# Kernel tuning notes

Hardware: AMD Instinct MI355X
Metric: run time of the kernel (lower is better)

## Reference

```python
import jax, jax.numpy as jnp
import numpy as np
import math

D_MODEL = 1024
N_HEADS = 16
D_K = D_MODEL // N_HEADS
R_TYPES = 8
B, S = 2, 2048


def setup_inputs() -> dict:
    key = jax.random.key(0)
    ks = jax.random.split(key, 12)
    sc = 0.02
    return {
        "x": jax.random.normal(ks[0], (B, S, D_MODEL), jnp.float32),
        "Wq": jax.random.normal(ks[1], (D_MODEL, D_MODEL), jnp.float32) * sc,
        "bq": jax.random.normal(ks[2], (D_MODEL,), jnp.float32) * sc,
        "Wk": jax.random.normal(ks[3], (D_MODEL, D_MODEL), jnp.float32) * sc,
        "bk": jax.random.normal(ks[4], (D_MODEL,), jnp.float32) * sc,
        "Wv": jax.random.normal(ks[5], (D_MODEL, D_MODEL), jnp.float32) * sc,
        "bv": jax.random.normal(ks[6], (D_MODEL,), jnp.float32) * sc,
        "Wo": jax.random.normal(ks[7], (D_MODEL, D_MODEL), jnp.float32) * sc,
        "bo": jax.random.normal(ks[8], (D_MODEL,), jnp.float32) * sc,
        "resource_bias": jax.random.normal(ks[9], (N_HEADS, R_TYPES, R_TYPES), jnp.float32),
        "resource_mask": jax.random.randint(ks[10], (B, S), 0, R_TYPES, jnp.int32),
        "attention_mask": jnp.ones((B, S), jnp.int32),
    }


def reference(x, resource_mask, attention_mask, Wq, bq, Wk, bk, Wv, bv, Wo, bo, resource_bias):
    # torch nn.Linear: y = x @ W.T + b
    def lin(h, W, b):
        return jnp.einsum("bsd,ed->bse", h, W) + b

    def split_heads(t):  # [B,S,D] -> [B,H,S,d_k]
        return t.reshape(B, S, N_HEADS, D_K).transpose(0, 2, 1, 3)

    Q = split_heads(lin(x, Wq, bq))
    K = split_heads(lin(x, Wk, bk))
    V = split_heads(lin(x, Wv, bv))

    scores = jnp.einsum("bhid,bhjd->bhij", Q, K) / math.sqrt(D_K)  # [B,H,S,S]

    # vectorized resource-bias gather: bias[h, r_i, r_j] added to scores[b,h,i,j]
    r = resource_mask.astype(jnp.int32)  # values guaranteed < R_TYPES
    # resource_bias[:, r[b,i], r[b,j]] -> [B,H,S,S]
    bias = resource_bias[:, r[:, :, None], r[:, None, :]]  # [H,B,S,S]
    scores = scores + bias.transpose(1, 0, 2, 3)

    mask = attention_mask[:, None, None, :]  # [B,1,1,S] broadcast to [B,H,S,S]
    scores = jnp.where(mask == 0, jnp.float32(-1e9), scores)

    attn = jax.nn.softmax(scores, axis=-1)  # dropout is identity in eval
    out = jnp.einsum("bhij,bhjd->bhid", attn, V)
    out = out.transpose(0, 2, 1, 3).reshape(B, S, D_MODEL)
    return jnp.einsum("bsd,ed->bse", out, Wo) + bo
```

## Files before the change

### kernel.cpp

```cpp
#include <hip/hip_runtime.h>
#include <cstdint>

#define D_MODEL 1024
#define NHEADS  16
#define DKH     64
#define SEQ     2048
#define NBATCH  2
#define MROWS   (NBATCH*SEQ)
#define RTYPES  8
#define LOG2E   1.44269504f

typedef __bf16 bf16;
typedef __bf16 bf16x4v __attribute__((ext_vector_type(4)));
typedef __bf16 bf16x8v __attribute__((ext_vector_type(8)));
typedef float  f32x4v  __attribute__((ext_vector_type(4)));

typedef unsigned int __attribute__((address_space(1))) as1_u32;
typedef unsigned int __attribute__((address_space(3))) as3_u32;

static __device__ __forceinline__ void gload_lds16(const void* g, void* l) {
  __builtin_amdgcn_global_load_lds((const as1_u32*)(uintptr_t)g,
                                   (as3_u32*)(uintptr_t)l, 16, 0, 0);
}

static __device__ __forceinline__ f32x4v mfma16(bf16x8v a, bf16x8v b, f32x4v c) {
  return __builtin_amdgcn_mfma_f32_16x16x32_bf16(a, b, c, 0, 0, 0);
}

__global__ void convert_kernel(const float* __restrict__ x,  const float* __restrict__ wq,
                               const float* __restrict__ wk, const float* __restrict__ wv,
                               const float* __restrict__ wo,
                               bf16* __restrict__ xb,  bf16* __restrict__ wqb,
                               bf16* __restrict__ wkb, bf16* __restrict__ wvb,
                               bf16* __restrict__ wob,
                               const float* __restrict__ rbias,
                               const int* __restrict__ rmask,
                               const int* __restrict__ amask,
                               float* __restrict__ biasg)
{
  int y = blockIdx.y;
  int i = blockIdx.x*256 + threadIdx.x;
  if (y == 0){
    float4 v = ((const float4*)x)[i];
    bf16x4v o = { (bf16)v.x, (bf16)v.y, (bf16)v.z, (bf16)v.w };
    ((bf16x4v*)xb)[i] = o;
  } else if (y < 5){
    if (i >= D_MODEL*D_MODEL/4) return;
    const float* src; bf16* dst;
    if (y == 1)      { src = wq; dst = wqb; }
    else if (y == 2) { src = wk; dst = wkb; }
    else if (y == 3) { src = wv; dst = wvb; }
    else             { src = wo; dst = wob; }
    float4 v = ((const float4*)src)[i];
    bf16x4v o = { (bf16)v.x, (bf16)v.y, (bf16)v.z, (bf16)v.w };
    ((bf16x4v*)dst)[i] = o;
  } else {
    if (i >= NHEADS*RTYPES*SEQ) return;
    #pragma unroll
    for (int bb=0; bb<NBATCH; bb++){
      int idx = bb*(NHEADS*RTYPES*SEQ) + i;
      int j  = idx & (SEQ-1);
      int t  = (idx >> 11) & 7;
      int hh = (idx >> 14) & 15;
      int rj = rmask[bb*SEQ + j];
      float am = amask[bb*SEQ + j] ? 0.f : -1e9f;
      biasg[idx] = (rbias[(hh*RTYPES + t)*RTYPES + rj] + am) * LOG2E;
    }
  }
}

struct GemmOuts { const bf16* W[3]; const float* bia[3]; void* out[3]; };

template<int FUSED>
__global__ __launch_bounds__(256, 3) void gemm_bt_kernel(
    const bf16* __restrict__ A, GemmOuts args, float qscale)
{
  const int K  = D_MODEL;
  const int z  = FUSED ? blockIdx.z : 0;
  const bf16*  Bw   = args.W[z];
  const float* bias = args.bia[z];
  void* outp        = args.out[z];
  const float scale = (FUSED && z==0) ? qscale : 1.0f;

  const int n0 = blockIdx.x*128, m0 = blockIdx.y*128;
  const int tid = threadIdx.x;
  const int w = tid>>6, lane = tid&63, g = lane>>4, c = lane&15;
  const int wm = w>>1, wn = w&1;

  __shared__ __align__(16) bf16 a_lds[2][128*32];
  __shared__ __align__(16) bf16 b_lds[2][128*32];

  const f32x4v fzero = {0.f,0.f,0.f,0.f};
  f32x4v acc[4][4];
  for (int i=0;i<4;i++) for (int j=0;j<4;j++) acc[i][j] = fzero;

  const int srow = tid>>2, sc8 = tid&3;

  auto STAGE = [&](int k0, int nb){
    gload_lds16(A  + (size_t)(m0+srow)*K     + k0 + sc8*8, &a_lds[nb][(w*64)*8]);
    gload_lds16(Bw + (size_t)(n0+srow)*K     + k0 + sc8*8, &b_lds[nb][(w*64)*8]);
    gload_lds16(A  + (size_t)(m0+64+srow)*K  + k0 + sc8*8, &a_lds[nb][(256 + w*64)*8]);
    gload_lds16(Bw + (size_t)(n0+64+srow)*K  + k0 + sc8*8, &b_lds[nb][(256 + w*64)*8]);
  };

  auto COMPUTE = [&](int nb){
    bf16x8v af[4], bfv[4];
    #pragma unroll
    for (int mt=0;mt<4;mt++)
      af[mt] = *(const bf16x8v*)&a_lds[nb][(wm*64 + mt*16 + c)*32 + g*8];
    #pragma unroll
    for (int nt=0;nt<4;nt++)
      bfv[nt] = *(const bf16x8v*)&b_lds[nb][(wn*64 + nt*16 + c)*32 + g*8];
    #pragma unroll
    for (int mt=0;mt<4;mt++)
      #pragma unroll
      for (int nt=0;nt<4;nt++)
        acc[mt][nt] = mfma16(af[mt], bfv[nt], acc[mt][nt]);
  };

  STAGE(0, 0);
  __syncthreads();
  int cur = 0;
  for (int k0=32; k0<K; k0+=32){
    STAGE(k0, cur^1);
    COMPUTE(cur);
    __syncthreads();
    cur ^= 1;
  }
  COMPUTE(cur);

  #pragma unroll
  for (int mt=0;mt<4;mt++){
    #pragma unroll
    for (int nt=0;nt<4;nt++){
      if (FUSED && z == 2){
        int m = m0 + wm*64 + mt*16 + g*4;
        int n = n0 + wn*64 + nt*16 + c;
        int bb=m>>11, s=m&2047, hh=n>>6, dk=n&63;
        float bn = bias[n];
        bf16x4v ov;
        #pragma unroll
        for (int r=0;r<4;r++) ov[r] = (bf16)(acc[mt][nt][r] + bn);
        *(bf16x4v*)&((bf16*)outp)[(((size_t)bb*NHEADS+hh)*DKH + dk)*SEQ + s] = ov;
      } else {
        #pragma unroll
        for (int r=0;r<4;r++){
          int m = m0 + wm*64 + mt*16 + g*4 + r;
          int n = n0 + wn*64 + nt*16 + c;
          float v = acc[mt][nt][r] + bias[n];
          if (FUSED){
            v *= scale;
            int bb=m>>11, s=m&2047, hh=n>>6, dk=n&63;
            ((bf16*)outp)[(((size_t)bb*NHEADS+hh)*SEQ + s)*DKH + dk] = (bf16)v;
          } else {
            ((float*)outp)[(size_t)m*D_MODEL + n] = v;
          }
        }
      }
    }
  }
}

__global__ __launch_bounds__(512, 4) void attn3_kernel(
    const bf16* __restrict__ Qg, const bf16* __restrict__ Kg,
    const bf16* __restrict__ Vtg, const float* __restrict__ biasg,
    const int* __restrict__ rmask, bf16* __restrict__ Og)
{
  const int b = blockIdx.z, h = blockIdx.y, q0 = blockIdx.x*128;
  const int tid = threadIdx.x;
  const int w = tid>>6, lane = tid&63, g = lane>>4, c = lane&15;
  const int bh = b*NHEADS + h;

  __shared__ __align__(16) bf16  k_lds[2][64*64];
  __shared__ __align__(16) bf16  vt_lds[2][64*64];
  __shared__ __align__(16) float bias_lds[2][8*64];

  const int qrow = q0 + w*16 + c;
  const bf16* qptr = Qg + ((size_t)bh*SEQ + qrow)*DKH;
  bf16x8v qf[2];
  qf[0] = *(const bf16x8v*)(qptr + g*8);
  qf[1] = *(const bf16x8v*)(qptr + 32 + g*8);

  const int tq = rmask[b*SEQ + qrow];
  const int tsw = (tq&7) << 2;

  f32x4v oacc[4];
  #pragma unroll
  for (int dt=0;dt<4;dt++) oacc[dt] = {0.f,0.f,0.f,0.f};
  float mrow = -1e30f, lrow = 0.f;

  const int rho = tid>>3;
  const int c8s = (tid&7) ^ (rho&7);
  const int jlog = ((rho>>4)&1)*32 + ((rho>>2)&3)*8 + ((rho>>5)&1)*4 + (rho&3);

  auto STAGE = [&](int j0, int nb){
    gload_lds16(Kg  + ((size_t)bh*SEQ + j0 + jlog)*DKH + (c8s<<3), &k_lds[nb][w*512]);
    gload_lds16(Vtg + ((size_t)bh*DKH + rho)*SEQ + j0 + (c8s<<3),  &vt_lds[nb][w*512]);
    if (w < 2){
      int chunk = w*64 + lane;
      int tcls = chunk>>4, c16 = chunk&15;
      int jsw = (c16<<2) ^ ((tcls&7)<<2);
      gload_lds16(biasg + ((size_t)(bh*RTYPES + tcls))*SEQ + j0 + jsw, &bias_lds[nb][w*256]);
    }
  };

  auto COMPUTE = [&](int nb){
    const char*  kb_ = (const char*)k_lds[nb];
    const char*  vb_ = (const char*)vt_lds[nb];
    const float* bb_ = &bias_lds[nb][0];

    f32x4v s[4];
    #pragma unroll
    for (int nt=0;nt<4;nt++){
      int jb = (nt&1)*32 + g*8 + (nt>>1)*4;
      s[nt] = *(const f32x4v*)&bb_[tq*64 + (jb ^ tsw)];
      #pragma unroll
      for (int kt=0;kt<2;kt++){
        int row = nt*16 + c;
        bf16x8v kf = *(const bf16x8v*)(kb_ + row*128 + ((kt*64 + g*16) ^ ((row&7)<<4)));
        s[nt] = mfma16(kf, qf[kt], s[nt]);
      }
    }

    float mx = s[0][0];
    #pragma unroll
    for (int nt=0;nt<4;nt++)
      #pragma unroll
      for (int r=0;r<4;r++) mx = fmaxf(mx, s[nt][r]);
    mx = fmaxf(mx, __shfl_xor(mx, 16));
    mx = fmaxf(mx, __shfl_xor(mx, 32));

    const bool skip = __all(mx - mrow <= 8.0f);
    const float mnew = skip ? mrow : fmaxf(mrow, mx);

    float sum = 0.f;
    #pragma unroll
    for (int nt=0;nt<4;nt++)
      #pragma unroll
      for (int r=0;r<4;r++){
        float p = exp2f(s[nt][r] - mnew);
        s[nt][r] = p;
        sum += p;
      }
    sum += __shfl_xor(sum, 16);
    sum += __shfl_xor(sum, 32);

    if (skip){
      lrow += sum;
    } else {
      float scl = exp2f(mrow - mnew);
      lrow = lrow*scl + sum;
      #pragma unroll
      for (int dt=0;dt<4;dt++)
        #pragma unroll
        for (int r=0;r<4;r++) oacc[dt][r] *= scl;
      mrow = mnew;
    }

    bf16x8v pa[2];
    #pragma unroll
    for (int kt=0;kt<2;kt++){
      pa[kt][0]=(bf16)s[kt][0];   pa[kt][1]=(bf16)s[kt][1];
      pa[kt][2]=(bf16)s[kt][2];   pa[kt][3]=(bf16)s[kt][3];
      pa[kt][4]=(bf16)s[kt+2][0]; pa[kt][5]=(bf16)s[kt+2][1];
      pa[kt][6]=(bf16)s[kt+2][2]; pa[kt][7]=(bf16)s[kt+2][3];
    }

    #pragma unroll
    for (int dt=0;dt<4;dt++){
      #pragma unroll
      for (int kt=0;kt<2;kt++){
        int vr = dt*16 + c;
        bf16x8v vf = *(const bf16x8v*)(vb_ + vr*128 + ((kt*64 + g*16) ^ ((vr&7)<<4)));
        oacc[dt] = mfma16(vf, pa[kt], oacc[dt]);
      }
    }
  };

  STAGE(0, 0);
  __syncthreads();
  int cur = 0;
  for (int t=0; t<SEQ/64; ++t){
    if (t+1 < SEQ/64) STAGE((t+1)*64, cur^1);
    COMPUTE(cur);
    __syncthreads();
    cur ^= 1;
  }

  const float inv = 1.0f / lrow;
  #pragma unroll
  for (int dt=0;dt<4;dt++){
    bf16x4v ov;
    #pragma unroll
    for (int r=0;r<4;r++) ov[r] = (bf16)(oacc[dt][r] * inv);
    int row = q0 + w*16 + c;
    int col = h*DKH + dt*16 + g*4;
    *(bf16x4v*)&Og[(size_t)(b*SEQ + row)*D_MODEL + col] = ov;
  }
}

extern "C" void kernel_launch(void* const* d_in, const int* in_sizes, int n_in,
                              void* d_out, int out_size, void* d_ws, size_t ws_size,
                              hipStream_t stream)
{
  (void)in_sizes; (void)n_in; (void)out_size; (void)ws_size;
  const float* x     = (const float*)d_in[0];
  const float* Wq    = (const float*)d_in[1];
  const float* bq    = (const float*)d_in[2];
  const float* Wk    = (const float*)d_in[3];
  const float* bk    = (const float*)d_in[4];
  const float* Wv    = (const float*)d_in[5];
  const float* bv    = (const float*)d_in[6];
  const float* Wo    = (const float*)d_in[7];
  const float* bo    = (const float*)d_in[8];
  const float* rbias = (const float*)d_in[9];
  const int*   rmask = (const int*)d_in[10];
  const int*   amask = (const int*)d_in[11];
  float* out = (float*)d_out;

  char* ws = (char*)d_ws;
  bf16*  xb    = (bf16*)(ws);
  bf16*  wqb   = (bf16*)(ws + (8u<<20));
  bf16*  wkb   = (bf16*)(ws + (10u<<20));
  bf16*  wvb   = (bf16*)(ws + (12u<<20));
  bf16*  wob   = (bf16*)(ws + (14u<<20));
  bf16*  qb    = (bf16*)(ws + (16u<<20));
  bf16*  kb    = (bf16*)(ws + (24u<<20));
  bf16*  vtb   = (bf16*)(ws + (32u<<20));
  bf16*  aob   = (bf16*)(ws + (40u<<20));
  float* biasg = (float*)(ws + (48u<<20));

  convert_kernel<<<dim3(4096,6), 256, 0, stream>>>(x,Wq,Wk,Wv,Wo, xb,wqb,wkb,wvb,wob,
                                                   rbias, rmask, amask, biasg);

  GemmOuts qkv;
  qkv.W[0]=wqb; qkv.W[1]=wkb; qkv.W[2]=wvb;
  qkv.bia[0]=bq; qkv.bia[1]=bk; qkv.bia[2]=bv;
  qkv.out[0]=qb; qkv.out[1]=kb; qkv.out[2]=vtb;
  gemm_bt_kernel<1><<<dim3(D_MODEL/128, MROWS/128, 3), 256, 0, stream>>>(xb, qkv, 0.125f*LOG2E);

  attn3_kernel<<<dim3(SEQ/128, NHEADS, NBATCH), 512, 0, stream>>>(qb, kb, vtb, biasg, rmask, aob);

  GemmOuts og;
  og.W[0]=wob; og.W[1]=wob; og.W[2]=wob;
  og.bia[0]=bo; og.bia[1]=bo; og.bia[2]=bo;
  og.out[0]=out; og.out[1]=out; og.out[2]=out;
  gemm_bt_kernel<0><<<dim3(D_MODEL/128, MROWS/128), 256, 0, stream>>>(aob, og, 1.0f);
}
```

Measured before the change: 142.3 us.

## Triple-buffer attention K/V loads with vmcnt waits and MFMA row sums

The attention kernel moves from double to triple buffering of K, V^T and bias tiles in LDS, prefetching two tiles ahead. The full __syncthreads is replaced by explicit s_waitcnt vmcnt counts plus a raw barrier, so the next tile's loads stay in flight across the barrier. The softmax row sum is now computed by an MFMA against a ones vector instead of VALU adds and cross-lane shuffles, and the max reduction is rewritten as a tree. The convert kernel is flattened to a 1D grid that launches no idle blocks. The costs are more LDS per block, which may reduce occupancy, and hand-counted vmcnt values that break if the number of loads per stage changes.

```diff
diff --git a/kernel.cpp b/kernel.cpp
--- a/kernel.cpp
+++ b/kernel.cpp
@@ -38,33 +38,33 @@
                                const int* __restrict__ amask,
                                float* __restrict__ biasg)
 {
-  int y = blockIdx.y;
-  int i = blockIdx.x*256 + threadIdx.x;
-  if (y == 0){
-    float4 v = ((const float4*)x)[i];
+  int idx = blockIdx.x*256 + threadIdx.x;
+  if (idx < 1048576){
+    float4 v = ((const float4*)x)[idx];
     bf16x4v o = { (bf16)v.x, (bf16)v.y, (bf16)v.z, (bf16)v.w };
-    ((bf16x4v*)xb)[i] = o;
-  } else if (y < 5){
-    if (i >= D_MODEL*D_MODEL/4) return;
+    ((bf16x4v*)xb)[idx] = o;
+  } else if (idx < 2097152){
+    int r = (idx - 1048576) >> 18;
+    int i = (idx - 1048576) & 262143;
     const float* src; bf16* dst;
-    if (y == 1)      { src = wq; dst = wqb; }
-    else if (y == 2) { src = wk; dst = wkb; }
-    else if (y == 3) { src = wv; dst = wvb; }
+    if (r == 0)      { src = wq; dst = wqb; }
+    else if (r == 1) { src = wk; dst = wkb; }
+    else if (r == 2) { src = wv; dst = wvb; }
     else             { src = wo; dst = wob; }
     float4 v = ((const float4*)src)[i];
     bf16x4v o = { (bf16)v.x, (bf16)v.y, (bf16)v.z, (bf16)v.w };
     ((bf16x4v*)dst)[i] = o;
   } else {
-    if (i >= NHEADS*RTYPES*SEQ) return;
+    int i = idx - 2097152;
     #pragma unroll
     for (int bb=0; bb<NBATCH; bb++){
-      int idx = bb*(NHEADS*RTYPES*SEQ) + i;
-      int j  = idx & (SEQ-1);
-      int t  = (idx >> 11) & 7;
-      int hh = (idx >> 14) & 15;
+      int id2 = bb*(NHEADS*RTYPES*SEQ) + i;
+      int j  = id2 & (SEQ-1);
+      int t  = (id2 >> 11) & 7;
+      int hh = (id2 >> 14) & 15;
       int rj = rmask[bb*SEQ + j];
       float am = amask[bb*SEQ + j] ? 0.f : -1e9f;
-      biasg[idx] = (rbias[(hh*RTYPES + t)*RTYPES + rj] + am) * LOG2E;
+      biasg[id2] = (rbias[(hh*RTYPES + t)*RTYPES + rj] + am) * LOG2E;
     }
   }
 }
@@ -161,7 +161,7 @@
   }
 }
 
-__global__ __launch_bounds__(512, 4) void attn3_kernel(
+__global__ __launch_bounds__(512, 4) void attn4_kernel(
     const bf16* __restrict__ Qg, const bf16* __restrict__ Kg,
     const bf16* __restrict__ Vtg, const float* __restrict__ biasg,
     const int* __restrict__ rmask, bf16* __restrict__ Og)
@@ -170,10 +170,11 @@
   const int tid = threadIdx.x;
   const int w = tid>>6, lane = tid&63, g = lane>>4, c = lane&15;
   const int bh = b*NHEADS + h;
-
-  __shared__ __align__(16) bf16  k_lds[2][64*64];
-  __shared__ __align__(16) bf16  vt_lds[2][64*64];
-  __shared__ __align__(16) float bias_lds[2][8*64];
+  const int NT = SEQ/64;
+
+  __shared__ __align__(16) bf16  k_lds[3][64*64];
+  __shared__ __align__(16) bf16  vt_lds[3][64*64];
+  __shared__ __align__(16) float bias_lds[3][8*64];
 
   const int qrow = q0 + w*16 + c;
   const bf16* qptr = Qg + ((size_t)bh*SEQ + qrow)*DKH;
@@ -184,10 +185,15 @@
   const int tq = rmask[b*SEQ + qrow];
   const int tsw = (tq&7) << 2;
 
+  bf16x8v ones;
+  #pragma unroll
+  for (int i=0;i<8;i++) ones[i] = (bf16)1.0f;
+
   f32x4v oacc[4];
   #pragma unroll
   for (int dt=0;dt<4;dt++) oacc[dt] = {0.f,0.f,0.f,0.f};
-  float mrow = -1e30f, lrow = 0.f;
+  f32x4v lacc = {0.f,0.f,0.f,0.f};
+  float mrow = -1e30f;
 
   const int rho = tid>>3;
   const int c8s = (tid&7) ^ (rho&7);
@@ -222,40 +228,32 @@
       }
     }
 
-    float mx = s[0][0];
-    #pragma unroll
-    for (int nt=0;nt<4;nt++)
-      #pragma unroll
-      for (int r=0;r<4;r++) mx = fmaxf(mx, s[nt][r]);
+    float a0 = fmaxf(fmaxf(s[0][0],s[0][1]),s[0][2]);
+    float a1 = fmaxf(fmaxf(s[0][3],s[1][0]),s[1][1]);
+    float a2 = fmaxf(fmaxf(s[1][2],s[1][3]),s[2][0]);
+    float a3 = fmaxf(fmaxf(s[2][1],s[2][2]),s[2][3]);
+    float a4 = fmaxf(fmaxf(s[3][0],s[3][1]),s[3][2]);
+    float mx = fmaxf(fmaxf(fmaxf(a0,a1),a2), fmaxf(fmaxf(a3,a4),s[3][3]));
     mx = fmaxf(mx, __shfl_xor(mx, 16));
     mx = fmaxf(mx, __shfl_xor(mx, 32));
 
-    const bool skip = __all(mx - mrow <= 8.0f);
-    const float mnew = skip ? mrow : fmaxf(mrow, mx);
-
-    float sum = 0.f;
-    #pragma unroll
-    for (int nt=0;nt<4;nt++)
-      #pragma unroll
-      for (int r=0;r<4;r++){
-        float p = exp2f(s[nt][r] - mnew);
-        s[nt][r] = p;
-        sum += p;
-      }
-    sum += __shfl_xor(sum, 16);
-    sum += __shfl_xor(sum, 32);
-
-    if (skip){
-      lrow += sum;
-    } else {
+    if (!__all(mx - mrow <= 8.0f)){
+      float mnew = fmaxf(mrow, mx);
       float scl = exp2f(mrow - mnew);
-      lrow = lrow*scl + sum;
       #pragma unroll
       for (int dt=0;dt<4;dt++)
         #pragma unroll
         for (int r=0;r<4;r++) oacc[dt][r] *= scl;
+      #pragma unroll
+      for (int r=0;r<4;r++) lacc[r] *= scl;
       mrow = mnew;
     }
+
+    #pragma unroll
+    for (int nt=0;nt<4;nt++)
+      #pragma unroll
+      for (int r=0;r<4;r++)
+        s[nt][r] = exp2f(s[nt][r] - mrow);
 
     bf16x8v pa[2];
     #pragma unroll
@@ -266,6 +264,9 @@
       pa[kt][6]=(bf16)s[kt+2][2]; pa[kt][7]=(bf16)s[kt+2][3];
     }
 
+    lacc = mfma16(ones, pa[0], lacc);
+    lacc = mfma16(ones, pa[1], lacc);
+
     #pragma unroll
     for (int dt=0;dt<4;dt++){
       #pragma unroll
@@ -278,16 +279,29 @@
   };
 
   STAGE(0, 0);
-  __syncthreads();
+  STAGE(64, 1);
+  if (w < 2) asm volatile("s_waitcnt vmcnt(3)" ::: "memory");
+  else       asm volatile("s_waitcnt vmcnt(2)" ::: "memory");
+  __builtin_amdgcn_s_barrier();
+
   int cur = 0;
-  for (int t=0; t<SEQ/64; ++t){
-    if (t+1 < SEQ/64) STAGE((t+1)*64, cur^1);
+  for (int t=0; t<NT; ++t){
+    if (t+2 < NT){
+      int nb2 = cur+2; if (nb2 >= 3) nb2 -= 3;
+      STAGE((t+2)*64, nb2);
+    }
     COMPUTE(cur);
-    __syncthreads();
-    cur ^= 1;
-  }
-
-  const float inv = 1.0f / lrow;
+    if (t+2 < NT){
+      if (w < 2) asm volatile("s_waitcnt vmcnt(3)" ::: "memory");
+      else       asm volatile("s_waitcnt vmcnt(2)" ::: "memory");
+    } else {
+      asm volatile("s_waitcnt vmcnt(0)" ::: "memory");
+    }
+    __builtin_amdgcn_s_barrier();
+    cur = (cur+1 == 3) ? 0 : cur+1;
+  }
+
+  const float inv = 1.0f / lacc[0];
   #pragma unroll
   for (int dt=0;dt<4;dt++){
     bf16x4v ov;
@@ -330,8 +344,8 @@
   bf16*  aob   = (bf16*)(ws + (40u<<20));
   float* biasg = (float*)(ws + (48u<<20));
 
-  convert_kernel<<<dim3(4096,6), 256, 0, stream>>>(x,Wq,Wk,Wv,Wo, xb,wqb,wkb,wvb,wob,
-                                                   rbias, rmask, amask, biasg);
+  convert_kernel<<<9216, 256, 0, stream>>>(x,Wq,Wk,Wv,Wo, xb,wqb,wkb,wvb,wob,
+                                           rbias, rmask, amask, biasg);
 
   GemmOuts qkv;
   qkv.W[0]=wqb; qkv.W[1]=wkb; qkv.W[2]=wvb;
@@ -339,7 +353,7 @@
   qkv.out[0]=qb; qkv.out[1]=kb; qkv.out[2]=vtb;
   gemm_bt_kernel<1><<<dim3(D_MODEL/128, MROWS/128, 3), 256, 0, stream>>>(xb, qkv, 0.125f*LOG2E);
 
-  attn3_kernel<<<dim3(SEQ/128, NHEADS, NBATCH), 512, 0, stream>>>(qb, kb, vtb, biasg, rmask, aob);
+  attn4_kernel<<<dim3(SEQ/128, NHEADS, NBATCH), 512, 0, stream>>>(qb, kb, vtb, biasg, rmask, aob);
 
   GemmOuts og;
   og.W[0]=wob; og.W[1]=wob; og.W[2]=wob;
```

Result: faster. 138.9 us (-2.4%).
